# Kernel tuning notes

Hardware: AMD Instinct MI355X
Metric: run time of the kernel (lower is better)

Reference implementation:

```python
import jax, jax.numpy as jnp
import numpy as np

SCALE = 0.0625      # spatial_scale
OUT = 7             # out_size (== part_size)
C_OUT = 256         # output_dim (== input channels, group_size=1)
SPP = 4             # sample_per_part
TRANS_STD = 0.1
FC_DIM = 1024
B, H, W = 4, 128, 128
N_ROI = 2000
IMG = 2048.0        # H / SCALE


def _round_half(x):
    # CUDA round(): half away from zero (coords are non-negative here)
    return jnp.floor(x + 0.5)


def deform_roi_pool(data, rois, offset):
    """Faithful port of deform_roi_pooling (DCNv2 deform PS-ROI pooling, group_size=1).
    data: [B,C,H,W]; rois: [N,5]; offset: None or [N,2,OUT,OUT]. Returns [N,C,OUT,OUT]."""
    Bn, C, Hh, Ww = data.shape
    N = rois.shape[0]
    b = rois[:, 0].astype(jnp.int32)
    sw = _round_half(rois[:, 1]) * SCALE - 0.5
    sh = _round_half(rois[:, 2]) * SCALE - 0.5
    ew = (_round_half(rois[:, 3]) + 1.0) * SCALE - 0.5
    eh = (_round_half(rois[:, 4]) + 1.0) * SCALE - 0.5
    rw = jnp.maximum(ew - sw, 0.1)
    rh = jnp.maximum(eh - sh, 0.1)
    bw, bh = rw / OUT, rh / OUT              # bin sizes
    subw, subh = bw / SPP, bh / SPP          # sub-bin sizes

    ph, pw = jnp.meshgrid(jnp.arange(OUT, dtype=data.dtype),
                          jnp.arange(OUT, dtype=data.dtype), indexing='ij')
    wstart = pw[None] * bw[:, None, None] + sw[:, None, None]   # [N,OUT,OUT]
    hstart = ph[None] * bh[:, None, None] + sh[:, None, None]
    if offset is not None:
        # part_size == out_size -> part index == bin index
        wstart = wstart + offset[:, 0] * TRANS_STD * rw[:, None, None]
        hstart = hstart + offset[:, 1] * TRANS_STD * rh[:, None, None]

    ih2, iw2 = jnp.meshgrid(jnp.arange(SPP, dtype=data.dtype),
                            jnp.arange(SPP, dtype=data.dtype), indexing='ij')
    ih2, iw2 = ih2.reshape(-1), iw2.reshape(-1)  # [SPP*SPP]
    # sample coords [S2, N, OUT, OUT]
    ws = wstart[None] + iw2[:, None, None, None] * subw[None, :, None, None]
    hs = hstart[None] + ih2[:, None, None, None] * subh[None, :, None, None]

    bb = b[:, None, None]  # [N,1,1]

    def body(carry, coords):
        acc, cnt = carry
        w, h = coords                                 # [N,OUT,OUT]
        valid = (w >= -0.5) & (w <= Ww - 0.5) & (h >= -0.5) & (h <= Hh - 0.5)
        wc = jnp.clip(w, 0.0, Ww - 1.0)
        hc = jnp.clip(h, 0.0, Hh - 1.0)
        x0 = jnp.floor(wc).astype(jnp.int32)
        y0 = jnp.floor(hc).astype(jnp.int32)
        x1 = jnp.minimum(x0 + 1, Ww - 1)
        y1 = jnp.minimum(y0 + 1, Hh - 1)
        dx = wc - x0
        dy = hc - y0
        v00 = data[bb, :, y0, x0]   # [N,OUT,OUT,C]
        v01 = data[bb, :, y0, x1]
        v10 = data[bb, :, y1, x0]
        v11 = data[bb, :, y1, x1]
        val = (((1 - dx) * (1 - dy))[..., None] * v00
               + (dx * (1 - dy))[..., None] * v01
               + ((1 - dx) * dy)[..., None] * v10
               + (dx * dy)[..., None] * v11)
        val = jnp.where(valid[..., None], val, 0.0)
        return (acc + val, cnt + valid.astype(data.dtype)), None

    init = (jnp.zeros((N, OUT, OUT, C), data.dtype),
            jnp.zeros((N, OUT, OUT), data.dtype))
    (s, cnt), _ = jax.lax.scan(body, init, (ws, hs))
    out = jnp.where(cnt[..., None] > 0, s / jnp.maximum(cnt, 1.0)[..., None], 0.0)
    return jnp.transpose(out, (0, 3, 1, 2))  # [N,C,OUT,OUT]


def setup_inputs() -> dict:
    key = jax.random.key(0)
    ks = jax.random.split(key, 16)
    data = jax.random.normal(ks[0], (B, C_OUT, H, W), dtype=jnp.float32)
    bidx = jax.random.randint(ks[1], (N_ROI,), 0, B).astype(jnp.float32)
    x1 = jax.random.uniform(ks[2], (N_ROI,), minval=0.0, maxval=IMG - 64.0)
    y1 = jax.random.uniform(ks[3], (N_ROI,), minval=0.0, maxval=IMG - 64.0)
    wbox = jax.random.uniform(ks[4], (N_ROI,), minval=16.0, maxval=400.0)
    hbox = jax.random.uniform(ks[5], (N_ROI,), minval=16.0, maxval=400.0)
    rois = jnp.stack([bidx, x1, y1,
                      jnp.minimum(x1 + wbox, IMG - 1.0),
                      jnp.minimum(y1 + hbox, IMG - 1.0)], axis=1)
    fin = OUT * OUT * C_OUT  # 12544
    def lin(k, i, o, s=None):
        s = (1.0 / np.sqrt(i)) if s is None else s
        return jax.random.normal(k, (i, o), dtype=jnp.float32) * s
    return {
        'data': data, 'rois': rois,
        'w1': lin(ks[6], fin, FC_DIM), 'b1': jnp.zeros((FC_DIM,), jnp.float32),
        'w2': lin(ks[7], FC_DIM, FC_DIM), 'b2': jnp.zeros((FC_DIM,), jnp.float32),
        'w3': lin(ks[8], FC_DIM, OUT * OUT * 2, 0.01), 'b3': jnp.zeros((OUT * OUT * 2,), jnp.float32),
        'mw1': lin(ks[9], fin, FC_DIM), 'mb1': jnp.zeros((FC_DIM,), jnp.float32),
        'mw2': lin(ks[10], FC_DIM, OUT * OUT, 0.01), 'mb2': jnp.zeros((OUT * OUT,), jnp.float32),
    }


def reference(data, rois, w1, b1, w2, b2, w3, b3, mw1, mb1, mw2, mb2):
    n = rois.shape[0]
    x = deform_roi_pool(data, rois, None)              # [N,C,OUT,OUT]
    xf = x.reshape(n, -1)
    h = jax.nn.relu(xf @ w1 + b1)
    h = jax.nn.relu(h @ w2 + b2)
    offset = (h @ w3 + b3).reshape(n, 2, OUT, OUT)
    m = jax.nn.relu(xf @ mw1 + mb1)
    mask = jax.nn.sigmoid(m @ mw2 + mb2).reshape(n, 1, OUT, OUT)
    feat = deform_roi_pool(data, rois, offset) * mask
    return feat
```

## Files before the change

kernel.cpp:

```cpp
#include <hip/hip_runtime.h>
#include <math.h>

#define WDIM 128
#define HDIM 128
#define BDIM 4
#define CDIM 256
#define NROI 2000
#define MPAD 2048
#define FIN  12544
#define FC   1024
#define HWC  (HDIM * WDIM * CDIM)

typedef unsigned short bf16r;
typedef unsigned short u16;
typedef __attribute__((ext_vector_type(8))) short bf16x8;
typedef __attribute__((ext_vector_type(4))) float f32x4;
typedef __attribute__((ext_vector_type(8))) _Float16 half8;
typedef __attribute__((ext_vector_type(8))) unsigned short ushort8v;

__device__ __forceinline__ bf16r f2bf(float f) {
    unsigned u = __float_as_uint(f);
    u += 0x7FFFu + ((u >> 16) & 1u);
    return (bf16r)(u >> 16);
}
__device__ __forceinline__ u16 f2h(float f) {
    union { u16 s; _Float16 h; } c; c.h = (_Float16)f; return c.s;
}

__device__ __forceinline__ void async16(const bf16r* g, bf16r* l) {
    __builtin_amdgcn_global_load_lds(
        (const __attribute__((address_space(1))) unsigned int*)g,
        (__attribute__((address_space(3))) unsigned int*)l, 16, 0, 0);
}

#define VMW(n) asm volatile("s_waitcnt vmcnt(" #n ")" ::: "memory")
#define BARRIER() __builtin_amdgcn_s_barrier()

__device__ __forceinline__ void roi_geom(const float* __restrict__ rois, int n,
                                         int& b, float& sw, float& sh,
                                         float& rw, float& rh) {
    const float* r = rois + (size_t)n * 5;
    b = (int)r[0];
    float r1 = floorf(r[1] + 0.5f);
    float r2 = floorf(r[2] + 0.5f);
    float r3 = floorf(r[3] + 0.5f);
    float r4 = floorf(r[4] + 0.5f);
    sw = r1 * 0.0625f - 0.5f;
    sh = r2 * 0.0625f - 0.5f;
    float ew = (r3 + 1.0f) * 0.0625f - 0.5f;
    float eh = (r4 + 1.0f) * 0.0625f - 0.5f;
    rw = fmaxf(ew - sw, 0.1f);
    rh = fmaxf(eh - sh, 0.1f);
}

__device__ __forceinline__ void build_geometry(
        int n, int tid, const float* __restrict__ rois,
        const float* __restrict__ offs,
        const float* __restrict__ maskb,
        float* axW, unsigned* axMeta, uint2* wpix, int* npx, float* scale) {
    if (tid < 98) {
        int po = tid >> 1, axis = tid & 1;
        int b; float sw, sh, rw, rh;
        roi_geom(rois, n, b, sw, sh, rw, rh);
        float bw = rw * (1.f / 7.f), bh = rh * (1.f / 7.f);
        int ph = po / 7, pw = po - ph * 7;
        float start, sub;
        if (axis == 0) {
            start = (float)pw * bw + sw;
            if (offs) start += offs[(size_t)n * 98 + po] * 0.1f * rw;
            sub = bw * 0.25f;
        } else {
            start = (float)ph * bh + sh;
            if (offs) start += offs[(size_t)n * 98 + 49 + po] * 0.1f * rh;
            sub = bh * 0.25f;
        }
        float wsl[5] = {0.f, 0.f, 0.f, 0.f, 0.f};
        int base = 0, cnt = 0, mx = 0, any = 0;
#pragma unroll
        for (int i = 0; i < 4; ++i) {
            float p = start + (float)i * sub;
            bool valid = (p >= -0.5f) & (p <= 127.5f);
            float pc = fminf(fmaxf(p, 0.f), 127.f);
            int p0 = (int)floorf(pc);
            float d = pc - (float)p0;
            int p1 = min(p0 + 1, 127);
            if (valid) {
                if (!any) { base = p0; any = 1; }
                int c0 = p0 - base, c1 = p1 - base;
                float w0 = 1.f - d;
#pragma unroll
                for (int k = 0; k < 5; ++k)
                    wsl[k] += ((c0 == k) ? w0 : 0.f) + ((c1 == k) ? d : 0.f);
                cnt++;
                mx = max(mx, c1);
            }
        }
        int N = any ? mx + 1 : 0;
        axMeta[tid] = (unsigned)(N | (cnt << 3) | (base << 6));
#pragma unroll
        for (int k = 0; k < 5; ++k) axW[tid * 5 + k] = wsl[k];
    }
    __syncthreads();
    if (tid < 245) {
        int po = tid / 5, r = tid - po * 5;
        unsigned mx_ = axMeta[po * 2], my_ = axMeta[po * 2 + 1];
        int NX = mx_ & 7, NY = my_ & 7;
        int bx = (mx_ >> 6) & 127, by = (my_ >> 6) & 127;
        if (r == 0) {
            int cntx = (mx_ >> 3) & 7, cnty = (my_ >> 3) & 7;
            int ct = cntx * cnty;
            float sc = (ct > 0) ? 1.f / (float)ct : 0.f;
            if (maskb) sc *= (ct > 0) ? maskb[(size_t)n * 49 + po] : 0.f;
            npx[po] = NX * NY;
            scale[po] = sc;
        }
        if (r < NY) {
            float wyr = axW[(po * 2 + 1) * 5 + r];
            unsigned rowoff = (unsigned)(((by + r) * 128 + bx) * 512);
#pragma unroll
            for (int c = 0; c < 5; ++c)
                if (c < NX)
                    wpix[po * 28 + r * NX + c] =
                        make_uint2(rowoff + (unsigned)c * 512u,
                                   __float_as_uint(wyr * axW[po * 2 * 5 + c]));
        }
    }
    __syncthreads();
}

__global__ __launch_bounds__(256) void transpose_kernel(const float* __restrict__ data,
                                                        u16* __restrict__ data_t) {
    __shared__ float t[32][33];
    int x0 = blockIdx.x << 5;
    int c0 = blockIdx.y << 5;
    int b  = blockIdx.z >> 7;
    int y  = blockIdx.z & 127;
    int tx = threadIdx.x, ty = threadIdx.y;
#pragma unroll
    for (int i = 0; i < 32; i += 8)
        t[ty + i][tx] = data[(((size_t)b * CDIM + c0 + ty + i) * HDIM + y) * WDIM + x0 + tx];
    __syncthreads();
#pragma unroll
    for (int i = 0; i < 32; i += 8)
        data_t[(((size_t)b * HDIM + y) * WDIM + x0 + ty + i) * CDIM + c0 + tx] = f2h(t[tx][ty + i]);
}

__global__ __launch_bounds__(256) void conv_kernel(const float* __restrict__ srcA,
                                                   const float* __restrict__ srcB,
                                                   int nsplit, int ncols, int Nout,
                                                   int K, int perm,
                                                   bf16r* __restrict__ dst) {
    __shared__ float t[32][33];
    int k0 = blockIdx.x << 5, n0 = blockIdx.y << 5;
    int tx = threadIdx.x & 31, ty = threadIdx.x >> 5;
#pragma unroll
    for (int i = 0; i < 32; i += 8) {
        int k = k0 + ty + i;
        int n = n0 + tx;
        const float* s = (n < nsplit) ? srcA : srcB;
        int col = (n < nsplit) ? n : n - nsplit;
        int row = perm ? ((k & 255) * 49 + (k >> 8)) : k;
        float v = (n < Nout && col < ncols) ? s[(size_t)row * ncols + col] : 0.f;
        t[ty + i][tx] = v;
    }
    __syncthreads();
#pragma unroll
    for (int i = 0; i < 32; i += 8) {
        int n = n0 + ty + i;
        if (n < Nout) dst[(size_t)n * K + k0 + tx] = f2bf(t[tx][ty + i]);
    }
}

__global__ __launch_bounds__(512) void pool1_kernel(const u16* __restrict__ data_t,
                                                    const float* __restrict__ rois,
                                                    bf16r* __restrict__ xf) {
    __shared__ ushort tileX[49][264];
    __shared__ float axW[98 * 5];
    __shared__ unsigned axMeta[98];
    __shared__ uint2 wpix[49 * 28];
    __shared__ int npx[49];
    __shared__ float scale[49];
    int n = blockIdx.x, tid = threadIdx.x;
    build_geometry(n, tid, rois, nullptr, nullptr, axW, axMeta, wpix, npx, scale);
    int b = (int)rois[(size_t)n * 5];
    int wave = tid >> 6, lane = tid & 63, shalf = lane >> 5, c8 = (lane & 31) << 3;
    const char* dpb = (const char*)(data_t + (size_t)b * HWC + c8);
    for (int po = wave * 2 + shalf; po < 49; po += 16) {
        int npe = npx[po];
        float sc = scale[po];
        const uint2* wp = wpix + po * 28;
        float a[8];
#pragma unroll
        for (int k = 0; k < 8; ++k) a[k] = 0.f;
        int p = 0;
        for (; p + 2 <= npe; p += 2) {
            uint2 q0 = wp[p], q1 = wp[p + 1];
            half8 v0 = *(const half8*)(dpb + q0.x);
            half8 v1 = *(const half8*)(dpb + q1.x);
            float w0 = __uint_as_float(q0.y), w1 = __uint_as_float(q1.y);
#pragma unroll
            for (int k = 0; k < 8; ++k) a[k] += w0 * (float)v0[k];
#pragma unroll
            for (int k = 0; k < 8; ++k) a[k] += w1 * (float)v1[k];
        }
        if (p < npe) {
            uint2 q0 = wp[p];
            half8 v0 = *(const half8*)(dpb + q0.x);
            float w0 = __uint_as_float(q0.y);
#pragma unroll
            for (int k = 0; k < 8; ++k) a[k] += w0 * (float)v0[k];
        }
        ushort8v o;
#pragma unroll
        for (int k = 0; k < 8; ++k) o[k] = f2bf(a[k] * sc);
        *(ushort8v*)&tileX[po][c8] = o;
    }
    __syncthreads();
    bf16r* xp = xf + (size_t)n * FIN;
    for (int u = tid; u < 3136; u += 512) {
        int k0 = u << 2;
        ushort4 o;
#pragma unroll
        for (int j = 0; j < 4; ++j) {
            int k = k0 + j;
            int c = k / 49;
            int po = k - c * 49;
            ((ushort*)&o)[j] = tileX[po][c];
        }
        *(ushort4*)(xp + k0) = o;
    }
}

__global__ __launch_bounds__(512) void pool2_kernel(const u16* __restrict__ data_t,
                                                    const float* __restrict__ rois,
                                                    const float* __restrict__ offs,
                                                    const float* __restrict__ maskb,
                                                    float* __restrict__ out) {
    __shared__ float tile[49 * 128];
    __shared__ float axW[98 * 5];
    __shared__ unsigned axMeta[98];
    __shared__ uint2 wpix[49 * 28];
    __shared__ int npx[49];
    __shared__ float scale[49];
    int n = blockIdx.x, chalf = blockIdx.y, tid = threadIdx.x;
    build_geometry(n, tid, rois, offs, maskb, axW, axMeta, wpix, npx, scale);
    int b = (int)rois[(size_t)n * 5];
    int wave = tid >> 6, lane = tid & 63, q = lane >> 4, c8 = (lane & 15) << 3;
    const char* dpb = (const char*)(data_t + (size_t)b * HWC + chalf * 128 + c8);
    for (int po = wave * 4 + q; po < 49; po += 32) {
        int npe = npx[po];
        float sc = scale[po];
        const uint2* wp = wpix + po * 28;
        float a[8];
#pragma unroll
        for (int k = 0; k < 8; ++k) a[k] = 0.f;
        int p = 0;
        for (; p + 2 <= npe; p += 2) {
            uint2 q0 = wp[p], q1 = wp[p + 1];
            half8 v0 = *(const half8*)(dpb + q0.x);
            half8 v1 = *(const half8*)(dpb + q1.x);
            float w0 = __uint_as_float(q0.y), w1 = __uint_as_float(q1.y);
#pragma unroll
            for (int k = 0; k < 8; ++k) a[k] += w0 * (float)v0[k];
#pragma unroll
            for (int k = 0; k < 8; ++k) a[k] += w1 * (float)v1[k];
        }
        if (p < npe) {
            uint2 q0 = wp[p];
            half8 v0 = *(const half8*)(dpb + q0.x);
            float w0 = __uint_as_float(q0.y);
#pragma unroll
            for (int k = 0; k < 8; ++k) a[k] += w0 * (float)v0[k];
        }
        int cs = c8 ^ ((po & 7) << 3);
        float4 lo = make_float4(a[0] * sc, a[1] * sc, a[2] * sc, a[3] * sc);
        float4 hi = make_float4(a[4] * sc, a[5] * sc, a[6] * sc, a[7] * sc);
        *(float4*)&tile[po * 128 + cs] = lo;
        *(float4*)&tile[po * 128 + cs + 4] = hi;
    }
    __syncthreads();
    float* op = out + (size_t)n * FIN + (size_t)chalf * 6272;
    for (int i = tid; i < 6272; i += 512) {
        int c = i / 49, po = i - c * 49;
        op[i] = tile[po * 128 + (c ^ ((po & 7) << 3))];
    }
}

#define STAGE_A(buf, h, kt) do { \
    async16(Abase + (size_t)(kt) * 64 + sAoff[h][0], &lds[buf][0][((h) * 128 + wave * 8) * 64]); \
    async16(Abase + (size_t)(kt) * 64 + sAoff[h][1], &lds[buf][0][((h) * 128 + 64 + wave * 8) * 64]); \
} while (0)
#define STAGE_B(buf, h, kt) do { \
    async16(Bbase + (size_t)(kt) * 64 + sBoff[h][0], &lds[buf][1][((h) * 128 + wave * 8) * 64]); \
    async16(Bbase + (size_t)(kt) * 64 + sBoff[h][1], &lds[buf][1][((h) * 128 + 64 + wave * 8) * 64]); \
} while (0)
#define LDA_HALF(buf, mh) do { \
    const char* Ar = (const char*)&lds[buf][0][0] + aQ + (mh) * 16384; \
    _Pragma("unroll") for (int i = 0; i < 4; ++i) \
        _Pragma("unroll") for (int ks = 0; ks < 2; ++ks) \
            aF[i][ks] = *(const bf16x8*)(Ar + i * 2048 + fRB[ks]); \
} while (0)
#define LDB_HALF(dst, buf, nh) do { \
    const char* Br = (const char*)&lds[buf][1][0] + bQ + (nh) * 16384; \
    _Pragma("unroll") for (int jf = 0; jf < 2; ++jf) \
        _Pragma("unroll") for (int ks = 0; ks < 2; ++ks) \
            dst[jf][ks] = *(const bf16x8*)(Br + jf * 2048 + fRB[ks]); \
} while (0)
#define MMA_Q(mh, nh, B) do { \
    __builtin_amdgcn_s_setprio(1); \
    _Pragma("unroll") for (int i = 0; i < 4; ++i) \
        _Pragma("unroll") for (int jf = 0; jf < 2; ++jf) \
            _Pragma("unroll") for (int ks = 0; ks < 2; ++ks) \
                acc[(mh) * 4 + i][(nh) * 2 + jf] = __builtin_amdgcn_mfma_f32_16x16x32_bf16( \
                    aF[i][ks], B[jf][ks], acc[(mh) * 4 + i][(nh) * 2 + jf], 0, 0, 0); \
    __builtin_amdgcn_s_setprio(0); \
} while (0)

__global__ __launch_bounds__(512, 2) void gemm256_kernel(
        const bf16r* __restrict__ A, int lda,
        const bf16r* __restrict__ Bt, int ldb,
        float* __restrict__ P, int Npad, int KS, int ktiles) {
    __shared__ bf16r lds[2][2][256 * 64];
    int tid = threadIdx.x;
    int wave = tid >> 6, lane = tid & 63;
    int l15 = lane & 15, quad = lane >> 4;
    int wm = wave >> 2, wn = wave & 3;

    int idx = blockIdx.x + gridDim.x * blockIdx.y;
    int nid = (idx & 7) * ((gridDim.x * gridDim.y) >> 3) + (idx >> 3);
    int bx = nid % gridDim.x, by = nid / gridDim.x;
    int m0 = by << 8, n0 = bx << 8;
    int z = blockIdx.z;

    int sAoff[2][2], sBoff[2][2];
#pragma unroll
    for (int h = 0; h < 2; ++h)
#pragma unroll
        for (int j = 0; j < 2; ++j) {
            int slot = h * 128 + j * 64 + wave * 8 + (lane >> 3);
            int g = (lane & 7) ^ ((slot >> 1) & 7);
            int rowA = ((slot >> 6) & 1) * 128 + (slot >> 7) * 64 + (slot & 63);
            int colB = ((slot >> 5) & 3) * 64 + (slot >> 7) * 32 + (slot & 31);
            sAoff[h][j] = rowA * lda + g * 8;
            sBoff[h][j] = colB * ldb + g * 8;
        }
    const bf16r* Abase = A + (size_t)m0 * lda;
    const bf16r* Bbase = Bt + (size_t)n0 * ldb;

    int fRB[2];
#pragma unroll
    for (int ks = 0; ks < 2; ++ks)
        fRB[ks] = l15 * 128 + ((((ks << 2) + quad) ^ ((l15 >> 1) & 7)) << 4);
    int aQ = wm * 8192;
    int bQ = wn * 4096;

    f32x4 acc[8][4];
#pragma unroll
    for (int i = 0; i < 8; ++i)
#pragma unroll
        for (int j = 0; j < 4; ++j) acc[i][j] = (f32x4){0.f, 0.f, 0.f, 0.f};
    bf16x8 aF[4][2], bF0[2][2], bF1[2][2];

    int tb = ((ktiles * z) / KS) & ~1;
    int te = (z == KS - 1) ? ktiles : ((ktiles * (z + 1)) / KS) & ~1;
    int nit = (te - tb) >> 1;

    STAGE_A(0, 0, tb); STAGE_B(0, 0, tb); STAGE_A(0, 1, tb); STAGE_B(0, 1, tb);
    STAGE_A(1, 0, tb + 1); STAGE_B(1, 0, tb + 1);
    VMW(4);
    BARRIER();

    for (int it = 0; it < nit; ++it) {
        int t1 = tb + 2 * it + 1, nx0 = t1 + 1, nx1 = t1 + 2;
        bool last = (it == nit - 1);
        LDA_HALF(0, 0); LDB_HALF(bF0, 0, 0);
        STAGE_A(1, 1, t1);
        BARRIER();
        MMA_Q(0, 0, bF0);
        BARRIER();

        LDB_HALF(bF1, 0, 1);
        STAGE_B(1, 1, t1);
        BARRIER();
        MMA_Q(0, 1, bF1);
        BARRIER();

        LDA_HALF(0, 1);
        if (!last) STAGE_A(0, 0, nx0);
        BARRIER();
        MMA_Q(1, 1, bF1);
        BARRIER();

        if (!last) STAGE_B(0, 0, nx0);
        BARRIER();
        MMA_Q(1, 0, bF0);
        if (last) { VMW(0); } else { VMW(4); }
        BARRIER();

        LDA_HALF(1, 0); LDB_HALF(bF0, 1, 0);
        if (!last) STAGE_A(0, 1, nx0);
        BARRIER();
        MMA_Q(0, 0, bF0);
        BARRIER();

        LDB_HALF(bF1, 1, 1);
        if (!last) STAGE_B(0, 1, nx0);
        BARRIER();
        MMA_Q(0, 1, bF1);
        BARRIER();

        LDA_HALF(1, 1);
        if (!last) STAGE_A(1, 0, nx1);
        BARRIER();
        MMA_Q(1, 1, bF1);
        BARRIER();

        if (!last) STAGE_B(1, 0, nx1);
        BARRIER();
        MMA_Q(1, 0, bF0);
        if (!last) { VMW(4); }
        BARRIER();
    }

    float* Pp = P + (size_t)z * MPAD * Npad;
#pragma unroll
    for (int I = 0; I < 8; ++I) {
        int row = m0 + wm * 128 + I * 16 + quad * 4;
#pragma unroll
        for (int J = 0; J < 4; ++J) {
            int col = n0 + wn * 64 + J * 16 + l15;
            float* o = Pp + (size_t)row * Npad + col;
#pragma unroll
            for (int r = 0; r < 4; ++r) o[(size_t)r * Npad] = acc[I][J][r];
        }
    }
}

__global__ __launch_bounds__(256) void gemm_mfma_kernel(
        const bf16r* __restrict__ A, int lda,
        const bf16r* __restrict__ Bt, int K,
        float* __restrict__ P, int Npad, int KS) {
    __shared__ bf16r As[128 * 32];
    __shared__ bf16r Bs[128 * 32];
    int tid = threadIdx.x;
    int wave = tid >> 6, lane = tid & 63;
    int nwgxy = gridDim.x * gridDim.y;
    int idx = blockIdx.x + gridDim.x * blockIdx.y;
    int chunk = nwgxy >> 3;
    int nid = (idx & 7) * chunk + (idx >> 3);
    int bx = nid % gridDim.x, by = nid / gridDim.x;
    int m0 = by << 7, n0 = bx << 7;
    int z = blockIdx.z;

    int srow = lane >> 2;
    int kchunk = ((lane & 3) ^ ((lane >> 3) & 3)) << 3;
    const bf16r* aG0 = A + (size_t)(m0 + wave * 32 + srow) * lda + kchunk;
    const bf16r* aG1 = A + (size_t)(m0 + wave * 32 + 16 + srow) * lda + kchunk;
    const bf16r* bG0 = Bt + (size_t)(n0 + wave * 32 + srow) * K + kchunk;
    const bf16r* bG1 = Bt + (size_t)(n0 + wave * 32 + 16 + srow) * K + kchunk;
    bf16r* aL0 = As + wave * 1024;
    bf16r* aL1 = As + wave * 1024 + 512;
    bf16r* bL0 = Bs + wave * 1024;
    bf16r* bL1 = Bs + wave * 1024 + 512;

    int l15 = lane & 15, quad = lane >> 4;
    int wr = wave >> 1, wc = wave & 1;
    int psw = (quad ^ ((l15 >> 1) & 3)) << 3;
    int aoff[4], boff[4];
#pragma unroll
    for (int t = 0; t < 4; ++t) {
        aoff[t] = ((wr * 64 + t * 16 + l15) * 32 + psw) * 2;
        boff[t] = ((wc * 64 + t * 16 + l15) * 32 + psw) * 2;
    }

    f32x4 acc[4][4];
#pragma unroll
    for (int i = 0; i < 4; ++i)
#pragma unroll
        for (int j = 0; j < 4; ++j) acc[i][j] = (f32x4){0.f, 0.f, 0.f, 0.f};

    int iters = K >> 5;
    int i0 = (int)((long)iters * z / KS);
    int i1 = (int)((long)iters * (z + 1) / KS);

    {
        size_t k0 = (size_t)i0 << 5;
        async16(aG0 + k0, aL0); async16(aG1 + k0, aL1);
        async16(bG0 + k0, bL0); async16(bG1 + k0, bL1);
    }
    for (int it = i0; it < i1; ++it) {
        __syncthreads();
        bf16x8 af[4], bfv[4];
#pragma unroll
        for (int t = 0; t < 4; ++t) af[t] = *(const bf16x8*)((const char*)As + aoff[t]);
#pragma unroll
        for (int t = 0; t < 4; ++t) bfv[t] = *(const bf16x8*)((const char*)Bs + boff[t]);
        __syncthreads();
        if (it + 1 < i1) {
            size_t k0 = (size_t)(it + 1) << 5;
            async16(aG0 + k0, aL0); async16(aG1 + k0, aL1);
            async16(bG0 + k0, bL0); async16(bG1 + k0, bL1);
        }
#pragma unroll
        for (int i = 0; i < 4; ++i)
#pragma unroll
            for (int j = 0; j < 4; ++j)
                acc[i][j] = __builtin_amdgcn_mfma_f32_16x16x32_bf16(af[i], bfv[j], acc[i][j], 0, 0, 0);
    }

    float* Pp = P + (size_t)z * MPAD * Npad;
#pragma unroll
    for (int i = 0; i < 4; ++i) {
        int row = m0 + wr * 64 + i * 16 + quad * 4;
#pragma unroll
        for (int j = 0; j < 4; ++j) {
            int col = n0 + wc * 64 + j * 16 + l15;
            float* o = Pp + (size_t)row * Npad + col;
#pragma unroll
            for (int r = 0; r < 4; ++r) o[(size_t)r * Npad] = acc[i][j][r];
        }
    }
}

__global__ __launch_bounds__(256) void reduce_kernel(
        const float* __restrict__ P, int shift, int KS,
        const float* __restrict__ bias0, const float* __restrict__ bias1, int bsplit,
        void* __restrict__ Out, int ldo, int M, int Nreal, int outmode) {
    int idx = (blockIdx.x * 256 + threadIdx.x) << 2;
    int Npad = 1 << shift;
    int row = idx >> shift, col = idx & (Npad - 1);
    f32x4 s = (f32x4){0.f, 0.f, 0.f, 0.f};
    size_t plane = (size_t)MPAD << shift;
    for (int zz = 0; zz < KS; ++zz) s += *(const f32x4*)(P + (size_t)zz * plane + idx);
    if (row < M) {
#pragma unroll
        for (int e = 0; e < 4; ++e) {
            int c = col + e;
            if (c < Nreal) {
                float b = (c < bsplit) ? bias0[c] : bias1[c - bsplit];
                float v = s[e] + b;
                if (outmode == 0) {
                    v = fmaxf(v, 0.f);
                    ((bf16r*)Out)[(size_t)row * ldo + c] = f2bf(v);
                } else {
                    if (outmode == 2) v = 1.f / (1.f + expf(-v));
                    ((float*)Out)[(size_t)row * ldo + c] = v;
                }
            }
        }
    }
}

extern "C" void kernel_launch(void* const* d_in, const int* in_sizes, int n_in,
                              void* d_out, int out_size, void* d_ws, size_t ws_size,
                              hipStream_t stream) {
    const float* data = (const float*)d_in[0];
    const float* rois = (const float*)d_in[1];
    const float* w1   = (const float*)d_in[2];
    const float* b1   = (const float*)d_in[3];
    const float* w2   = (const float*)d_in[4];
    const float* b2   = (const float*)d_in[5];
    const float* w3   = (const float*)d_in[6];
    const float* b3   = (const float*)d_in[7];
    const float* mw1  = (const float*)d_in[8];
    const float* mb1  = (const float*)d_in[9];
    const float* mw2  = (const float*)d_in[10];
    const float* mb2  = (const float*)d_in[11];
    float* out = (float*)d_out;

    char* w = (char*)d_ws;
    size_t off = 0;
    auto carve = [&](size_t bytes) {
        void* p = w + off;
        off += (bytes + 255) & ~(size_t)255;
        return p;
    };
    u16* data_t   = (u16*)carve((size_t)BDIM * HDIM * WDIM * CDIM * 2);
    bf16r* xf     = (bf16r*)carve((size_t)MPAD * FIN * 2);
    bf16r* bt1    = (bf16r*)carve((size_t)MPAD * FIN * 2);
    bf16r* hm     = (bf16r*)carve((size_t)MPAD * 2048 * 2);
    bf16r* h2     = (bf16r*)carve((size_t)MPAD * 1024 * 2);
    bf16r* bt2    = (bf16r*)carve((size_t)1024 * 1024 * 2);
    bf16r* bt3    = (bf16r*)carve((size_t)128 * 1024 * 2);
    bf16r* bt4    = (bf16r*)carve((size_t)128 * 1024 * 2);
    float* offs   = (float*)carve((size_t)NROI * 98 * 4);
    float* maskb  = (float*)carve((size_t)NROI * 49 * 4);
    float* P      = (float*)(w + off);
    size_t plane  = (size_t)MPAD * 2048 * 4;
    size_t avail  = (ws_size > off) ? ws_size - off : 0;
    int use256 = (avail >= 4 * plane);

    conv_kernel<<<dim3(392, 64), 256, 0, stream>>>(w1, mw1, 1024, 1024, 2048, FIN, 0, bt1);
    conv_kernel<<<dim3(32, 32), 256, 0, stream>>>(w2, w2, 1 << 30, 1024, 1024, 1024, 0, bt2);
    conv_kernel<<<dim3(32, 4), 256, 0, stream>>>(w3, w3, 1 << 30, 98, 98, 1024, 0, bt3);
    conv_kernel<<<dim3(32, 2), 256, 0, stream>>>(mw2, mw2, 1 << 30, 49, 49, 1024, 0, bt4);
    transpose_kernel<<<dim3(4, 8, 512), dim3(32, 8), 0, stream>>>(data, data_t);
    pool1_kernel<<<dim3(NROI), 512, 0, stream>>>(data_t, rois, xf);

    if (use256) {
        gemm256_kernel<<<dim3(8, 8, 4), 512, 0, stream>>>(xf, FIN, bt1, FIN, P, 2048, 4, 196);
        reduce_kernel<<<4096, 256, 0, stream>>>(P, 11, 4, b1, mb1, 1024, hm, 2048, NROI, 2048, 0);
        gemm256_kernel<<<dim3(4, 8, 8), 512, 0, stream>>>(hm, 2048, bt2, 1024, P, 1024, 8, 16);
        reduce_kernel<<<2048, 256, 0, stream>>>(P, 10, 8, b2, b2, 1 << 30, h2, 1024, NROI, 1024, 0);
    } else {
        gemm_mfma_kernel<<<dim3(16, 16, 3), 256, 0, stream>>>(xf, FIN, bt1, FIN, P, 2048, 3);
        reduce_kernel<<<4096, 256, 0, stream>>>(P, 11, 3, b1, mb1, 1024, hm, 2048, NROI, 2048, 0);
        gemm_mfma_kernel<<<dim3(8, 16, 4), 256, 0, stream>>>(hm, 2048, bt2, 1024, P, 1024, 4);
        reduce_kernel<<<2048, 256, 0, stream>>>(P, 10, 4, b2, b2, 1 << 30, h2, 1024, NROI, 1024, 0);
    }
    gemm_mfma_kernel<<<dim3(1, 16, 8), 256, 0, stream>>>(h2, 1024, bt3, 1024, P, 128, 8);
    reduce_kernel<<<256, 256, 0, stream>>>(P, 7, 8, b3, b3, 1 << 30, offs, 98, NROI, 98, 1);
    gemm_mfma_kernel<<<dim3(1, 16, 8), 256, 0, stream>>>(hm + 1024, 2048, bt4, 1024, P, 128, 8);
    reduce_kernel<<<256, 256, 0, stream>>>(P, 7, 8, mb2, mb2, 1 << 30, maskb, 49, NROI, 49, 2);

    pool2_kernel<<<dim3(NROI, 2), 512, 0, stream>>>(data_t, rois, offs, maskb, out);
}
```

Before: 526.9 us.

## Merge prep kernels, store split-K partials as bf16, batch tail GEMMs

Merges the four weight-conversion kernels and the data transpose into one prep kernel, which removes several launches. Splits the first FC GEMM's partial sums are now stored in bf16 instead of fp32, halving the traffic of the partial-sum write and the reduction read, at some cost in accumulation precision. The second GEMM now always runs the smaller gemm_mfma path with 4 splits. The offset and mask head GEMMs run in one batched launch followed by one combined reduce kernel.

```diff
diff --git a/kernel.cpp b/kernel.cpp
--- a/kernel.cpp
+++ b/kernel.cpp
@@ -22,6 +22,9 @@
     unsigned u = __float_as_uint(f);
     u += 0x7FFFu + ((u >> 16) & 1u);
     return (bf16r)(u >> 16);
+}
+__device__ __forceinline__ float bf2f(bf16r h) {
+    return __uint_as_float(((unsigned)h) << 16);
 }
 __device__ __forceinline__ u16 f2h(float f) {
     union { u16 s; _Float16 h; } c; c.h = (_Float16)f; return c.s;
@@ -128,39 +131,20 @@
     __syncthreads();
 }
 
-__global__ __launch_bounds__(256) void transpose_kernel(const float* __restrict__ data,
-                                                        u16* __restrict__ data_t) {
-    __shared__ float t[32][33];
-    int x0 = blockIdx.x << 5;
-    int c0 = blockIdx.y << 5;
-    int b  = blockIdx.z >> 7;
-    int y  = blockIdx.z & 127;
-    int tx = threadIdx.x, ty = threadIdx.y;
-#pragma unroll
-    for (int i = 0; i < 32; i += 8)
-        t[ty + i][tx] = data[(((size_t)b * CDIM + c0 + ty + i) * HDIM + y) * WDIM + x0 + tx];
-    __syncthreads();
-#pragma unroll
-    for (int i = 0; i < 32; i += 8)
-        data_t[(((size_t)b * HDIM + y) * WDIM + x0 + ty + i) * CDIM + c0 + tx] = f2h(t[tx][ty + i]);
-}
-
-__global__ __launch_bounds__(256) void conv_kernel(const float* __restrict__ srcA,
-                                                   const float* __restrict__ srcB,
-                                                   int nsplit, int ncols, int Nout,
-                                                   int K, int perm,
-                                                   bf16r* __restrict__ dst) {
-    __shared__ float t[32][33];
-    int k0 = blockIdx.x << 5, n0 = blockIdx.y << 5;
-    int tx = threadIdx.x & 31, ty = threadIdx.x >> 5;
+__device__ __forceinline__ void conv_body(const float* __restrict__ srcA,
+                                          const float* __restrict__ srcB,
+                                          int nsplit, int ncols, int Nout, int K,
+                                          int kb, int nb, bf16r* __restrict__ dst,
+                                          float (*t)[33], int tid) {
+    int k0 = kb << 5, n0 = nb << 5;
+    int tx = tid & 31, ty = tid >> 5;
 #pragma unroll
     for (int i = 0; i < 32; i += 8) {
         int k = k0 + ty + i;
         int n = n0 + tx;
         const float* s = (n < nsplit) ? srcA : srcB;
         int col = (n < nsplit) ? n : n - nsplit;
-        int row = perm ? ((k & 255) * 49 + (k >> 8)) : k;
-        float v = (n < Nout && col < ncols) ? s[(size_t)row * ncols + col] : 0.f;
+        float v = (n < Nout && col < ncols) ? s[(size_t)k * ncols + col] : 0.f;
         t[ty + i][tx] = v;
     }
     __syncthreads();
@@ -168,6 +152,52 @@
     for (int i = 0; i < 32; i += 8) {
         int n = n0 + ty + i;
         if (n < Nout) dst[(size_t)n * K + k0 + tx] = f2bf(t[tx][ty + i]);
+    }
+}
+
+__global__ __launch_bounds__(256) void prep_kernel(
+        const float* __restrict__ w1, const float* __restrict__ mw1,
+        const float* __restrict__ w2, const float* __restrict__ w3,
+        const float* __restrict__ mw2,
+        bf16r* __restrict__ bt1, bf16r* __restrict__ bt2,
+        bf16r* __restrict__ bt3, bf16r* __restrict__ bt4,
+        const float* __restrict__ data, u16* __restrict__ data_t) {
+    __shared__ float t[32][33];
+    int tid = threadIdx.x;
+    int blk = blockIdx.x;
+    if (blk < 25088) {
+        conv_body(w1, mw1, 1024, 1024, 2048, FIN, blk % 392, blk / 392, bt1, t, tid);
+        return;
+    }
+    blk -= 25088;
+    if (blk < 1024) {
+        conv_body(w2, w2, 1 << 30, 1024, 1024, 1024, blk & 31, blk >> 5, bt2, t, tid);
+        return;
+    }
+    blk -= 1024;
+    if (blk < 128) {
+        conv_body(w3, w3, 1 << 30, 98, 98, 1024, blk & 31, blk >> 5, bt3, t, tid);
+        return;
+    }
+    blk -= 128;
+    if (blk < 64) {
+        conv_body(mw2, mw2, 1 << 30, 49, 49, 1024, blk & 31, blk >> 5, bt4, t, tid);
+        return;
+    }
+    blk -= 64;
+    {
+        int x0 = (blk & 3) << 5;
+        int c0 = ((blk >> 2) & 7) << 5;
+        int bz = blk >> 5;
+        int b = bz >> 7, y = bz & 127;
+        int tx = tid & 31, ty = tid >> 5;
+#pragma unroll
+        for (int i = 0; i < 32; i += 8)
+            t[ty + i][tx] = data[(((size_t)b * CDIM + c0 + ty + i) * HDIM + y) * WDIM + x0 + tx];
+        __syncthreads();
+#pragma unroll
+        for (int i = 0; i < 32; i += 8)
+            data_t[(((size_t)b * HDIM + y) * WDIM + x0 + ty + i) * CDIM + c0 + tx] = f2h(t[tx][ty + i]);
     }
 }
 
@@ -319,7 +349,7 @@
 __global__ __launch_bounds__(512, 2) void gemm256_kernel(
         const bf16r* __restrict__ A, int lda,
         const bf16r* __restrict__ Bt, int ldb,
-        float* __restrict__ P, int Npad, int KS, int ktiles) {
+        bf16r* __restrict__ P, int Npad, int KS, int ktiles) {
     __shared__ bf16r lds[2][2][256 * 64];
     int tid = threadIdx.x;
     int wave = tid >> 6, lane = tid & 63;
@@ -422,16 +452,16 @@
         BARRIER();
     }
 
-    float* Pp = P + (size_t)z * MPAD * Npad;
+    bf16r* Pp = P + (size_t)z * MPAD * Npad;
 #pragma unroll
     for (int I = 0; I < 8; ++I) {
         int row = m0 + wm * 128 + I * 16 + quad * 4;
 #pragma unroll
         for (int J = 0; J < 4; ++J) {
             int col = n0 + wn * 64 + J * 16 + l15;
-            float* o = Pp + (size_t)row * Npad + col;
-#pragma unroll
-            for (int r = 0; r < 4; ++r) o[(size_t)r * Npad] = acc[I][J][r];
+            bf16r* o = Pp + (size_t)row * Npad + col;
+#pragma unroll
+            for (int r = 0; r < 4; ++r) o[(size_t)r * Npad] = f2bf(acc[I][J][r]);
         }
     }
 }
@@ -522,8 +552,95 @@
     }
 }
 
+__global__ __launch_bounds__(256) void gemm_tail_kernel(
+        const bf16r* __restrict__ A0, int lda0,
+        const bf16r* __restrict__ A1, int lda1,
+        const bf16r* __restrict__ Bt0, const bf16r* __restrict__ Bt1,
+        float* __restrict__ P) {
+    __shared__ bf16r As[128 * 32];
+    __shared__ bf16r Bs[128 * 32];
+    int tid = threadIdx.x;
+    int wave = tid >> 6, lane = tid & 63;
+    int prob = blockIdx.y >> 4;
+    int m0 = (blockIdx.y & 15) << 7;
+    const bf16r* A = prob ? A1 : A0;
+    int lda = prob ? lda1 : lda0;
+    const bf16r* Bt = prob ? Bt1 : Bt0;
+    int z = blockIdx.z;
+    const int K = 1024, KS = 8, Npad = 128;
+
+    int srow = lane >> 2;
+    int kchunk = ((lane & 3) ^ ((lane >> 3) & 3)) << 3;
+    const bf16r* aG0 = A + (size_t)(m0 + wave * 32 + srow) * lda + kchunk;
+    const bf16r* aG1 = A + (size_t)(m0 + wave * 32 + 16 + srow) * lda + kchunk;
+    const bf16r* bG0 = Bt + (size_t)(wave * 32 + srow) * K + kchunk;
+    const bf16r* bG1 = Bt + (size_t)(wave * 32 + 16 + srow) * K + kchunk;
+    bf16r* aL0 = As + wave * 1024;
+    bf16r* aL1 = As + wave * 1024 + 512;
+    bf16r* bL0 = Bs + wave * 1024;
+    bf16r* bL1 = Bs + wave * 1024 + 512;
+
+    int l15 = lane & 15, quad = lane >> 4;
+    int wr = wave >> 1, wc = wave & 1;
+    int psw = (quad ^ ((l15 >> 1) & 3)) << 3;
+    int aoff[4], boff[4];
+#pragma unroll
+    for (int t = 0; t < 4; ++t) {
+        aoff[t] = ((wr * 64 + t * 16 + l15) * 32 + psw) * 2;
+        boff[t] = ((wc * 64 + t * 16 + l15) * 32 + psw) * 2;
+    }
+
+    f32x4 acc[4][4];
+#pragma unroll
+    for (int i = 0; i < 4; ++i)
+#pragma unroll
+        for (int j = 0; j < 4; ++j) acc[i][j] = (f32x4){0.f, 0.f, 0.f, 0.f};
+
+    int iters = K >> 5;
+    int i0 = iters * z / KS;
+    int i1 = iters * (z + 1) / KS;
+
+    {
+        size_t k0 = (size_t)i0 << 5;
+        async16(aG0 + k0, aL0); async16(aG1 + k0, aL1);
+        async16(bG0 + k0, bL0); async16(bG1 + k0, bL1);
+    }
+    for (int it = i0; it < i1; ++it) {
+        __syncthreads();
+        bf16x8 af[4], bfv[4];
+#pragma unroll
+        for (int t = 0; t < 4; ++t) af[t] = *(const bf16x8*)((const char*)As + aoff[t]);
+#pragma unroll
+        for (int t = 0; t < 4; ++t) bfv[t] = *(const bf16x8*)((const char*)Bs + boff[t]);
+        __syncthreads();
+        if (it + 1 < i1) {
+            size_t k0 = (size_t)(it + 1) << 5;
+            async16(aG0 + k0, aL0); async16(aG1 + k0, aL1);
+            async16(bG0 + k0, bL0); async16(bG1 + k0, bL1);
+        }
+#pragma unroll
+        for (int i = 0; i < 4; ++i)
+#pragma unroll
+            for (int j = 0; j < 4; ++j)
+                acc[i][j] = __builtin_amdgcn_mfma_f32_16x16x32_bf16(af[i], bfv[j], acc[i][j], 0, 0, 0);
+    }
+
+    float* Pp = P + (size_t)(prob * 8 + z) * (MPAD * 128);
+#pragma unroll
+    for (int i = 0; i < 4; ++i) {
+        int row = m0 + wr * 64 + i * 16 + quad * 4;
+#pragma unroll
+        for (int j = 0; j < 4; ++j) {
+            int col = wc * 64 + j * 16 + l15;
+            float* o = Pp + (size_t)row * Npad + col;
+#pragma unroll
+            for (int r = 0; r < 4; ++r) o[(size_t)r * Npad] = acc[i][j][r];
+        }
+    }
+}
+
 __global__ __launch_bounds__(256) void reduce_kernel(
-        const float* __restrict__ P, int shift, int KS,
+        const void* __restrict__ Pv, int shift, int KS, int pbf16,
         const float* __restrict__ bias0, const float* __restrict__ bias1, int bsplit,
         void* __restrict__ Out, int ldo, int M, int Nreal, int outmode) {
     int idx = (blockIdx.x * 256 + threadIdx.x) << 2;
@@ -531,7 +648,16 @@
     int row = idx >> shift, col = idx & (Npad - 1);
     f32x4 s = (f32x4){0.f, 0.f, 0.f, 0.f};
     size_t plane = (size_t)MPAD << shift;
-    for (int zz = 0; zz < KS; ++zz) s += *(const f32x4*)(P + (size_t)zz * plane + idx);
+    if (pbf16) {
+        const bf16r* P = (const bf16r*)Pv;
+        for (int zz = 0; zz < KS; ++zz) {
+            ushort4 u = *(const ushort4*)(P + (size_t)zz * plane + idx);
+            s[0] += bf2f(u.x); s[1] += bf2f(u.y); s[2] += bf2f(u.z); s[3] += bf2f(u.w);
+        }
+    } else {
+        const float* P = (const float*)Pv;
+        for (int zz = 0; zz < KS; ++zz) s += *(const f32x4*)(P + (size_t)zz * plane + idx);
+    }
     if (row < M) {
 #pragma unroll
         for (int e = 0; e < 4; ++e) {
@@ -546,6 +672,35 @@
                     if (outmode == 2) v = 1.f / (1.f + expf(-v));
                     ((float*)Out)[(size_t)row * ldo + c] = v;
                 }
+            }
+        }
+    }
+}
+
+__global__ __launch_bounds__(256) void reduce34_kernel(
+        const float* __restrict__ P, const float* __restrict__ b3,
+        const float* __restrict__ mb2, float* __restrict__ offs,
+        float* __restrict__ maskb) {
+    int blk = blockIdx.x;
+    int prob = blk >> 8;
+    int idx = ((blk & 255) * 256 + threadIdx.x) << 2;
+    int row = idx >> 7, col = idx & 127;
+    f32x4 s = (f32x4){0.f, 0.f, 0.f, 0.f};
+    size_t plane = (size_t)MPAD * 128;
+    const float* Pb = P + (size_t)(prob * 8) * plane;
+    for (int zz = 0; zz < 8; ++zz) s += *(const f32x4*)(Pb + (size_t)zz * plane + idx);
+    if (row < NROI) {
+        if (prob == 0) {
+#pragma unroll
+            for (int e = 0; e < 4; ++e) {
+                int c = col + e;
+                if (c < 98) offs[(size_t)row * 98 + c] = s[e] + b3[c];
+            }
+        } else {
+#pragma unroll
+            for (int e = 0; e < 4; ++e) {
+                int c = col + e;
+                if (c < 49) maskb[(size_t)row * 49 + c] = 1.f / (1.f + expf(-(s[e] + mb2[c])));
             }
         }
     }
@@ -585,33 +740,33 @@
     bf16r* bt4    = (bf16r*)carve((size_t)128 * 1024 * 2);
     float* offs   = (float*)carve((size_t)NROI * 98 * 4);
     float* maskb  = (float*)carve((size_t)NROI * 49 * 4);
-    float* P      = (float*)(w + off);
+    void*  P      = (void*)(w + off);
     size_t plane  = (size_t)MPAD * 2048 * 4;
     size_t avail  = (ws_size > off) ? ws_size - off : 0;
     int use256 = (avail >= 4 * plane);
 
-    conv_kernel<<<dim3(392, 64), 256, 0, stream>>>(w1, mw1, 1024, 1024, 2048, FIN, 0, bt1);
-    conv_kernel<<<dim3(32, 32), 256, 0, stream>>>(w2, w2, 1 << 30, 1024, 1024, 1024, 0, bt2);
-    conv_kernel<<<dim3(32, 4), 256, 0, stream>>>(w3, w3, 1 << 30, 98, 98, 1024, 0, bt3);
-    conv_kernel<<<dim3(32, 2), 256, 0, stream>>>(mw2, mw2, 1 << 30, 49, 49, 1024, 0, bt4);
-    transpose_kernel<<<dim3(4, 8, 512), dim3(32, 8), 0, stream>>>(data, data_t);
+    prep_kernel<<<42688, 256, 0, stream>>>(w1, mw1, w2, w3, mw2,
+                                           bt1, bt2, bt3, bt4, data, data_t);
     pool1_kernel<<<dim3(NROI), 512, 0, stream>>>(data_t, rois, xf);
 
     if (use256) {
-        gemm256_kernel<<<dim3(8, 8, 4), 512, 0, stream>>>(xf, FIN, bt1, FIN, P, 2048, 4, 196);
-        reduce_kernel<<<4096, 256, 0, stream>>>(P, 11, 4, b1, mb1, 1024, hm, 2048, NROI, 2048, 0);
-        gemm256_kernel<<<dim3(4, 8, 8), 512, 0, stream>>>(hm, 2048, bt2, 1024, P, 1024, 8, 16);
-        reduce_kernel<<<2048, 256, 0, stream>>>(P, 10, 8, b2, b2, 1 << 30, h2, 1024, NROI, 1024, 0);
+        gemm256_kernel<<<dim3(8, 8, 4), 512, 0, stream>>>(xf, FIN, bt1, FIN,
+                                                          (bf16r*)P, 2048, 4, 196);
+        reduce_kernel<<<4096, 256, 0, stream>>>(P, 11, 4, 1, b1, mb1, 1024,
+                                                hm, 2048, NROI, 2048, 0);
     } else {
-        gemm_mfma_kernel<<<dim3(16, 16, 3), 256, 0, stream>>>(xf, FIN, bt1, FIN, P, 2048, 3);
-        reduce_kernel<<<4096, 256, 0, stream>>>(P, 11, 3, b1, mb1, 1024, hm, 2048, NROI, 2048, 0);
-        gemm_mfma_kernel<<<dim3(8, 16, 4), 256, 0, stream>>>(hm, 2048, bt2, 1024, P, 1024, 4);
-        reduce_kernel<<<2048, 256, 0, stream>>>(P, 10, 4, b2, b2, 1 << 30, h2, 1024, NROI, 1024, 0);
-    }
-    gemm_mfma_kernel<<<dim3(1, 16, 8), 256, 0, stream>>>(h2, 1024, bt3, 1024, P, 128, 8);
-    reduce_kernel<<<256, 256, 0, stream>>>(P, 7, 8, b3, b3, 1 << 30, offs, 98, NROI, 98, 1);
-    gemm_mfma_kernel<<<dim3(1, 16, 8), 256, 0, stream>>>(hm + 1024, 2048, bt4, 1024, P, 128, 8);
-    reduce_kernel<<<256, 256, 0, stream>>>(P, 7, 8, mb2, mb2, 1 << 30, maskb, 49, NROI, 49, 2);
+        gemm_mfma_kernel<<<dim3(16, 16, 3), 256, 0, stream>>>(xf, FIN, bt1, FIN,
+                                                              (float*)P, 2048, 3);
+        reduce_kernel<<<4096, 256, 0, stream>>>(P, 11, 3, 0, b1, mb1, 1024,
+                                                hm, 2048, NROI, 2048, 0);
+    }
+    gemm_mfma_kernel<<<dim3(8, 16, 4), 256, 0, stream>>>(hm, 2048, bt2, 1024,
+                                                         (float*)P, 1024, 4);
+    reduce_kernel<<<2048, 256, 0, stream>>>(P, 10, 4, 0, b2, b2, 1 << 30,
+                                            h2, 1024, NROI, 1024, 0);
+    gemm_tail_kernel<<<dim3(1, 32, 8), 256, 0, stream>>>(h2, 1024, hm + 1024, 2048,
+                                                         bt3, bt4, (float*)P);
+    reduce34_kernel<<<512, 256, 0, stream>>>((const float*)P, b3, mb2, offs, maskb);
 
     pool2_kernel<<<dim3(NROI, 2), 512, 0, stream>>>(data_t, rois, offs, maskb, out);
 }
```

Result: faster. 483.6 us (-8.2%).
